# Performance work log

Hardware: AMD Instinct MI355X
Metric: run time of the kernel (lower is better)

The kernel has to match this reference:

```python
import jax, jax.numpy as jnp
import numpy as np

OUTPUT_LENGTH = 2048  # init_kwargs: output_length


def setup_inputs() -> dict:
    key = jax.random.key(0)
    k1, k2 = jax.random.split(key)
    B, N, C = 16, 512, 512
    encoder_output = jax.random.normal(k1, (B, N, C), dtype=jnp.float32)
    log_durations = jax.random.normal(k2, (B, N, 1), dtype=jnp.float32)
    return {"encoder_output": encoder_output, "log_durations": log_durations}


def _alignment(log_durations, max_length):
    # log_durations: (B, N, 1) -> durations (B, N), matching the numpy uint8 math:
    # dur = uint8(2^log + 1e-4) * (log > 0); uint8 cast truncates (values stay < 256 here).
    ld = log_durations[..., 0]                                   # (B, N)
    mask = (ld > 0)
    dur = (jnp.floor(jnp.power(2.0, ld) + 1e-4)).astype(jnp.int32) * mask.astype(jnp.int32)
    ends = jnp.cumsum(dur, axis=1)                               # (B, N) inclusive cumsum
    starts = ends - dur                                          # exclusive cumsum
    t = jnp.arange(max_length, dtype=jnp.int32)                  # (L,)
    # align[b, t, p] = 1 iff starts[b,p] <= t < ends[b,p]
    align = (t[None, :, None] >= starts[:, None, :]) & (t[None, :, None] < ends[:, None, :])
    return align.astype(jnp.float32)                             # (B, L, N)


def reference(encoder_output, log_durations):
    align = _alignment(log_durations, OUTPUT_LENGTH)             # (B, L, N)
    # (B, L, N) @ (B, N, C) -> (B, L, C)
    return jnp.einsum('bln,bnc->blc', align, encoder_output)
```

## Files before the change

### kernel.cpp

```cpp
#include <hip/hip_runtime.h>

#define B_SZ 16
#define N_SZ 512
#define C_SZ 512
#define L_SZ 2048

__global__ __launch_bounds__(N_SZ) void build_idx_kernel(
    const float* __restrict__ log_durations,
    int* __restrict__ idx)
{
    __shared__ int s[N_SZ];
    const int b = blockIdx.x;
    const int n = threadIdx.x;

    const float ld = log_durations[b * N_SZ + n];
    int dur = 0;
    if (ld > 0.0f) dur = (int)floorf(exp2f(ld) + 1e-4f);

    s[n] = dur;
    __syncthreads();
    #pragma unroll
    for (int off = 1; off < N_SZ; off <<= 1) {
        int add = (n >= off) ? s[n - off] : 0;
        __syncthreads();
        s[n] += add;
        __syncthreads();
    }

    const int end   = s[n];
    const int start = end - dur;

    if (start < L_SZ) {
        const int e = min(end, L_SZ);
        for (int t = start; t < e; ++t) idx[b * L_SZ + t] = n;
    }

    const int total = min(s[N_SZ - 1], L_SZ);
    for (int t = total + n; t < L_SZ; t += N_SZ) idx[b * L_SZ + t] = -1;
}

__global__ __launch_bounds__(C_SZ / 4) void gather_kernel(
    const float4* __restrict__ enc,
    const int*    __restrict__ idx,
    float4*       __restrict__ out)
{
    const int row = blockIdx.x;
    const int b   = row >> 11;
    const int p   = idx[row];
    const int c4  = threadIdx.x;

    float4 v;
    if (p >= 0) {
        v = enc[(size_t)(b * N_SZ + p) * (C_SZ / 4) + c4];
    } else {
        v = make_float4(0.f, 0.f, 0.f, 0.f);
    }
    out[(size_t)row * (C_SZ / 4) + c4] = v;
}

extern "C" void kernel_launch(void* const* d_in, const int* in_sizes, int n_in,
                              void* d_out, int out_size, void* d_ws, size_t ws_size,
                              hipStream_t stream) {
    const float* enc = (const float*)d_in[0];
    const float* ld  = (const float*)d_in[1];
    float* out       = (float*)d_out;
    int* idx         = (int*)d_ws;

    build_idx_kernel<<<B_SZ, N_SZ, 0, stream>>>(ld, idx);
    gather_kernel<<<B_SZ * L_SZ, C_SZ / 4, 0, stream>>>(
        (const float4*)enc, idx, (float4*)out);
}
```

Baseline: 85.58 us.

## Use wavefront shuffle scan and grid-stride gather with fewer blocks

The duration prefix sum now uses a per-wavefront shuffle scan plus a small shared-memory reduction across waves, which removes the many block-wide barriers. The gather kernel changes from one 128-thread block per output row to a fixed grid of 2048 blocks of 256 threads. Each thread handles 8 unrolled float4 elements, with more loads in flight per thread. The aim is to cut scan latency and block-scheduling overhead for the 64MB output write, at the cost of repeated idx loads per element.

```diff
diff --git a/kernel.cpp b/kernel.cpp
--- a/kernel.cpp
+++ b/kernel.cpp
@@ -4,30 +4,40 @@
 #define N_SZ 512
 #define C_SZ 512
 #define L_SZ 2048
+#define ROW4 (C_SZ / 4)
+#define TOTAL4 (B_SZ * L_SZ * ROW4)
 
 __global__ __launch_bounds__(N_SZ) void build_idx_kernel(
     const float* __restrict__ log_durations,
     int* __restrict__ idx)
 {
-    __shared__ int s[N_SZ];
-    const int b = blockIdx.x;
-    const int n = threadIdx.x;
+    __shared__ int wsum[8];
+    const int b    = blockIdx.x;
+    const int n    = threadIdx.x;
+    const int lane = n & 63;
+    const int w    = n >> 6;
 
     const float ld = log_durations[b * N_SZ + n];
     int dur = 0;
     if (ld > 0.0f) dur = (int)floorf(exp2f(ld) + 1e-4f);
 
-    s[n] = dur;
+    int scan = dur;
+    #pragma unroll
+    for (int o = 1; o < 64; o <<= 1) {
+        int v = __shfl_up(scan, o, 64);
+        if (lane >= o) scan += v;
+    }
+    if (lane == 63) wsum[w] = scan;
     __syncthreads();
+
+    int base = 0, total = 0;
     #pragma unroll
-    for (int off = 1; off < N_SZ; off <<= 1) {
-        int add = (n >= off) ? s[n - off] : 0;
-        __syncthreads();
-        s[n] += add;
-        __syncthreads();
+    for (int i = 0; i < 8; ++i) {
+        const int s = wsum[i];
+        if (i < w) base += s;
+        total += s;
     }
-
-    const int end   = s[n];
+    const int end   = base + scan;
     const int start = end - dur;
 
     if (start < L_SZ) {
@@ -35,27 +45,32 @@
         for (int t = start; t < e; ++t) idx[b * L_SZ + t] = n;
     }
 
-    const int total = min(s[N_SZ - 1], L_SZ);
-    for (int t = total + n; t < L_SZ; t += N_SZ) idx[b * L_SZ + t] = -1;
+    const int tmin = min(total, L_SZ);
+    for (int t = tmin + n; t < L_SZ; t += N_SZ) idx[b * L_SZ + t] = -1;
 }
 
-__global__ __launch_bounds__(C_SZ / 4) void gather_kernel(
+#define G_BLOCKS 2048
+#define G_THREADS 256
+#define G_STRIDE (G_BLOCKS * G_THREADS)
+#define G_ITERS (TOTAL4 / G_STRIDE)
+
+__global__ __launch_bounds__(G_THREADS) void gather_kernel(
     const float4* __restrict__ enc,
     const int*    __restrict__ idx,
     float4*       __restrict__ out)
 {
-    const int row = blockIdx.x;
-    const int b   = row >> 11;
-    const int p   = idx[row];
-    const int c4  = threadIdx.x;
-
-    float4 v;
-    if (p >= 0) {
-        v = enc[(size_t)(b * N_SZ + p) * (C_SZ / 4) + c4];
-    } else {
-        v = make_float4(0.f, 0.f, 0.f, 0.f);
+    const int g0 = blockIdx.x * G_THREADS + threadIdx.x;
+    #pragma unroll
+    for (int it = 0; it < G_ITERS; ++it) {
+        const int g   = g0 + it * G_STRIDE;
+        const int row = g >> 7;
+        const int b   = row >> 11;
+        const int c4  = g & (ROW4 - 1);
+        const int p   = idx[row];
+        float4 v = make_float4(0.f, 0.f, 0.f, 0.f);
+        if (p >= 0) v = enc[(size_t)((b << 9) + p) * ROW4 + c4];
+        out[g] = v;
     }
-    out[(size_t)row * (C_SZ / 4) + c4] = v;
 }
 
 extern "C" void kernel_launch(void* const* d_in, const int* in_sizes, int n_in,
@@ -67,6 +82,6 @@
     int* idx         = (int*)d_ws;
 
     build_idx_kernel<<<B_SZ, N_SZ, 0, stream>>>(ld, idx);
-    gather_kernel<<<B_SZ * L_SZ, C_SZ / 4, 0, stream>>>(
+    gather_kernel<<<G_BLOCKS, G_THREADS, 0, stream>>>(
         (const float4*)enc, idx, (float4*)out);
 }
```

New measurement: 83.26 us. 1.03x faster.
